# Optimization experiments

Measured on AMD Instinct MI355X. Metric: run time of the kernel, lower is better.

Reference implementation:

```python
import jax, jax.numpy as jnp
import numpy as np

ACT_BITS = 8
W_BITS = 8
C_IN = 64


def round_ste(x):
    # straight-through rounding (Brevitas training behavior)
    return x + jax.lax.stop_gradient(jnp.round(x) - x)


def fake_quant(x, scale, bits, signed):
    if signed:
        lo, hi = -(2 ** (bits - 1)), 2 ** (bits - 1) - 1
    else:
        lo, hi = 0, 2 ** bits - 1
    return jnp.clip(round_ste(x / scale), lo, hi) * scale


def conv_nchw(x, w, pad, groups=1):
    return jax.lax.conv_general_dilated(
        x, w, window_strides=(1, 1), padding=((pad, pad), (pad, pad)),
        dimension_numbers=("NCHW", "OIHW", "NCHW"), feature_group_count=groups)


def setup_inputs() -> dict:
    key = jax.random.key(0)
    k0, k1, k2, k3 = jax.random.split(key, 4)
    x = jax.random.normal(k0, (8, 64, 112, 112), jnp.float32)
    w1 = jax.random.normal(k1, (64, 1, 3, 3), jnp.float32) * 0.05    # depthwise 3x3
    w2 = jax.random.normal(k2, (128, 64, 1, 1), jnp.float32) * 0.05  # pointwise 1x1
    w_sc = jax.random.normal(k3, (128, 64, 1, 1), jnp.float32) * 0.05  # shortcut 1x1
    sc = lambda v: jnp.asarray(v, jnp.float32)
    return dict(x=x, w1=w1, w2=w2, w_sc=w_sc,
                s_in=sc(0.03), s_relu=sc(0.02), s_add=sc(0.03),
                sw1=sc(0.004), sw2=sc(0.004), sw_sc=sc(0.004))


def reference(x, w1, w2, w_sc, s_in, s_relu, s_add, sw1, sw2, sw_sc):
    # quant_input: signed 8-bit fake-quant of the activation
    xq = fake_quant(x, s_in, ACT_BITS, True)
    # shortcut: 1x1 conv with int8 fake-quantized weights (inplane != ouplane)
    identity = conv_nchw(xq, fake_quant(w_sc, sw_sc, W_BITS, True), pad=0)
    # conv1: depthwise 3x3 (groups=inplane) with int8 fake-quantized weights
    y = conv_nchw(xq, fake_quant(w1, sw1, W_BITS, True), pad=1, groups=C_IN)
    # relu2: QuantReLU -> unsigned 8-bit fake-quant of relu
    y = fake_quant(jax.nn.relu(y), s_relu, ACT_BITS, False)
    # conv2: pointwise 1x1
    y = conv_nchw(y, fake_quant(w2, sw2, W_BITS, True), pad=0)
    # residual_add: add then requantize to signed 8-bit
    return fake_quant(y + identity, s_add, ACT_BITS, True)
```

## Files before the change

kernel.cpp:

```cpp
#include <hip/hip_runtime.h>
#include <hip/hip_bf16.h>
#include <stdint.h>

#define NIMG 8
#define CIN  64
#define HWI  12544
#define NP   100352
#define COUT 128

typedef short v8s __attribute__((ext_vector_type(8)));
typedef float v4f __attribute__((ext_vector_type(4)));

static __device__ __forceinline__ int q8(float x, float inv, float lo, float hi) {
    float t = rintf(x * inv);
    t = fminf(fmaxf(t, lo), hi);
    return (int)t;
}

static __device__ __forceinline__ uint32_t funnel(uint32_t hi, uint32_t lo, int sh) {
    return (uint32_t)(((((uint64_t)hi) << 32) | (uint64_t)lo) >> sh);
}

static __device__ __forceinline__ int dot4(uint32_t a, uint32_t b, int c) {
    int acc = c;
    #pragma unroll
    for (int i = 0; i < 4; ++i)
        acc += (int)(int8_t)(a >> (8*i)) * (int)(int8_t)(b >> (8*i));
    return acc;
}

static __device__ __forceinline__ uint16_t i2bf(int v) {
    union { float f; uint32_t u; } c; c.f = (float)v;
    return (uint16_t)(c.u >> 16);
}

__global__ void __launch_bounds__(256) wprep_kernel(
    const float* __restrict__ w2, const float* __restrict__ wsc,
    const float* __restrict__ sw2p, const float* __restrict__ swscp,
    uint16_t* __restrict__ wbuf)
{
    int t = blockIdx.x * 256 + threadIdx.x;
    int f = t * 4;
    int co = f >> 6, k = f & 63;
    float inv2 = 1.0f / sw2p[0];
    float invs = 1.0f / swscp[0];
    float4 a = *(const float4*)(w2 + f);
    float4 b = *(const float4*)(wsc + f);
    float av[4] = {a.x, a.y, a.z, a.w};
    float bv[4] = {b.x, b.y, b.z, b.w};
    uint16_t* d2 = wbuf + co*128 + k;
    uint16_t* ds = wbuf + co*128 + 64 + k;
    ushort2 p2a = make_ushort2(i2bf(q8(av[0], inv2, -128.f, 127.f)),
                               i2bf(q8(av[1], inv2, -128.f, 127.f)));
    ushort2 p2b = make_ushort2(i2bf(q8(av[2], inv2, -128.f, 127.f)),
                               i2bf(q8(av[3], inv2, -128.f, 127.f)));
    ushort2 psa = make_ushort2(i2bf(q8(bv[0], invs, -128.f, 127.f)),
                               i2bf(q8(bv[1], invs, -128.f, 127.f)));
    ushort2 psb = make_ushort2(i2bf(q8(bv[2], invs, -128.f, 127.f)),
                               i2bf(q8(bv[3], invs, -128.f, 127.f)));
    *(ushort2*)(d2)     = p2a;  *(ushort2*)(d2 + 2) = p2b;
    *(ushort2*)(ds)     = psa;  *(ushort2*)(ds + 2) = psb;
}

__global__ void __launch_bounds__(256) dwq_kernel(
    const float* __restrict__ x, const float* __restrict__ w1,
    const float* __restrict__ sinp, const float* __restrict__ srelup,
    const float* __restrict__ sw1p,
    uint16_t* __restrict__ act)
{
    __shared__ int8_t tile[64 * 468];
    int bid = blockIdx.x;
    int n = bid / 56, ht = bid - n*56, hb = ht*2;
    int tid = threadIdx.x;
    float sin_f = sinp[0];
    float inv_sin = 1.0f / sin_f;

    for (int i = 0; i < 28; ++i) {
        int id = tid + i*256;
        int c = id / 112; int rem = id - c*112;
        int r = rem / 28; int seg = rem - r*28;
        int grow = hb + r - 1;
        float4 v = make_float4(0.f, 0.f, 0.f, 0.f);
        if ((unsigned)grow < 112u)
            v = *(const float4*)(x + ((size_t)(n*64 + c) * HWI + grow*112 + seg*4));
        float vv[4] = {v.x, v.y, v.z, v.w};
        uint32_t pk = 0;
        #pragma unroll
        for (int e = 0; e < 4; ++e) {
            int q = q8(vv[e], inv_sin, -128.0f, 127.0f);
            pk |= (uint32_t)(q & 255) << (8*e);
        }
        *(uint32_t*)&tile[c*468 + r*116 + seg*4] = pk;
    }
    {
        int c = tid >> 2, r = tid & 3;
        *(uint32_t*)&tile[c*468 + r*116 + 112] = 0;
    }
    __syncthreads();

    int wave = tid >> 6, lane = tid & 63;
    int rsel = wave >> 1;
    int row  = hb + rsel;
    int half = wave & 1;
    int c = lane;

    float isw1 = 1.0f / sw1p[0];
    uint32_t wp[3];
    #pragma unroll
    for (int ky = 0; ky < 3; ++ky) {
        uint32_t pk = 0;
        #pragma unroll
        for (int kx = 0; kx < 3; ++kx) {
            int q = q8(w1[c*9 + ky*3 + kx], isw1, -128.0f, 127.0f);
            pk |= (uint32_t)(q & 255) << (8*kx);
        }
        wp[ky] = pk;
    }
    float r1 = (sin_f * sw1p[0]) / srelup[0];

    int base[3];
    #pragma unroll
    for (int r2 = 0; r2 < 3; ++r2) base[r2] = c*468 + (rsel + r2)*116;
    int w0b = 56*half;

    uint32_t Ar[3], Br[3], Cr[3];
    #pragma unroll
    for (int r2 = 0; r2 < 3; ++r2) {
        Ar[r2] = half ? *(uint32_t*)&tile[base[r2] + w0b - 4] : 0u;
        Br[r2] = *(uint32_t*)&tile[base[r2] + w0b];
        Cr[r2] = *(uint32_t*)&tile[base[r2] + w0b + 4];
    }
    size_t pbase = (size_t)n*HWI + (size_t)row*112 + w0b;

    for (int q = 0; q < 14; ++q) {
        int acc0 = 0, acc1 = 0, acc2 = 0, acc3 = 0;
        #pragma unroll
        for (int r2 = 0; r2 < 3; ++r2) {
            uint32_t d0 = funnel(Br[r2], Ar[r2], 24);
            uint32_t d1 = Br[r2];
            uint32_t d2 = funnel(Cr[r2], Br[r2], 8);
            uint32_t d3 = funnel(Cr[r2], Br[r2], 16);
            acc0 = dot4(d0, wp[r2], acc0);
            acc1 = dot4(d1, wp[r2], acc1);
            acc2 = dot4(d2, wp[r2], acc2);
            acc3 = dot4(d3, wp[r2], acc3);
        }
        int accs[4] = {acc0, acc1, acc2, acc3};
        uint32_t xdw = Br[1];
        uint16_t* ap = act + (pbase + (size_t)q*4)*128 + c;
        #pragma unroll
        for (int j = 0; j < 4; ++j) {
            float t = rintf((float)accs[j] * r1);
            t = fminf(fmaxf(t, 0.0f), 255.0f);
            int xv = (int)(int8_t)((xdw >> (8*j)) & 255);
            ap[(size_t)j*128]      = i2bf((int)t);
            ap[(size_t)j*128 + 64] = i2bf(xv);
        }
        #pragma unroll
        for (int r2 = 0; r2 < 3; ++r2) { Ar[r2] = Br[r2]; Br[r2] = Cr[r2]; }
        if (q < 13) {
            #pragma unroll
            for (int r2 = 0; r2 < 3; ++r2)
                Cr[r2] = *(uint32_t*)&tile[base[r2] + w0b + q*4 + 8];
        }
    }
}

__global__ void __launch_bounds__(256) gemm_kernel(
    const uint16_t* __restrict__ act, const uint16_t* __restrict__ wbuf,
    const float* __restrict__ sinp, const float* __restrict__ srelup,
    const float* __restrict__ saddp, const float* __restrict__ sw2p,
    const float* __restrict__ swscp,
    float* __restrict__ out)
{
    int bid = blockIdx.x;
    int tid = threadIdx.x;
    int wave = tid >> 6, lane = tid & 63;
    int lr = lane >> 4, ln = lane & 15;
    int p0 = bid * 128;
    int nimg = bid / 98;
    int hw0 = (bid - nimg*98) * 128;

    float S2  = sw2p[0] * srelup[0];
    float Ssc = swscp[0] * sinp[0];
    float sadd = saddp[0];
    float inv_sadd = 1.0f / sadd;

    v8s a[2][4];
    #pragma unroll
    for (int mi = 0; mi < 2; ++mi) {
        int m = (wave*2 + mi)*16 + ln;
        #pragma unroll
        for (int seg = 0; seg < 4; ++seg)
            a[mi][seg] = *(const v8s*)(wbuf + (size_t)m*128 + seg*32 + lr*8);
    }

    for (int nt = 0; nt < 8; ++nt) {
        const uint16_t* bp = act + (size_t)(p0 + nt*16 + ln)*128 + lr*8;
        v8s bf[4];
        #pragma unroll
        for (int seg = 0; seg < 4; ++seg)
            bf[seg] = *(const v8s*)(bp + seg*32);
        int px = hw0 + nt*16 + ln;
        #pragma unroll
        for (int mi = 0; mi < 2; ++mi) {
            v4f acc2 = {0.f, 0.f, 0.f, 0.f};
            v4f accs = {0.f, 0.f, 0.f, 0.f};
            acc2 = __builtin_amdgcn_mfma_f32_16x16x32_bf16(a[mi][0], bf[0], acc2, 0, 0, 0);
            acc2 = __builtin_amdgcn_mfma_f32_16x16x32_bf16(a[mi][1], bf[1], acc2, 0, 0, 0);
            accs = __builtin_amdgcn_mfma_f32_16x16x32_bf16(a[mi][2], bf[2], accs, 0, 0, 0);
            accs = __builtin_amdgcn_mfma_f32_16x16x32_bf16(a[mi][3], bf[3], accs, 0, 0, 0);
            size_t obase = ((size_t)nimg*COUT + (size_t)(wave*2 + mi)*16 + lr*4) * HWI + px;
            #pragma unroll
            for (int r = 0; r < 4; ++r) {
                float v = S2 * acc2[r] + Ssc * accs[r];
                float t = rintf(v * inv_sadd);
                t = fminf(fmaxf(t, -128.0f), 127.0f);
                out[obase + (size_t)r*HWI] = t * sadd;
            }
        }
    }
}

extern "C" void kernel_launch(void* const* d_in, const int* in_sizes, int n_in,
                              void* d_out, int out_size, void* d_ws, size_t ws_size,
                              hipStream_t stream) {
    const float* x     = (const float*)d_in[0];
    const float* w1    = (const float*)d_in[1];
    const float* w2    = (const float*)d_in[2];
    const float* wsc   = (const float*)d_in[3];
    const float* sin   = (const float*)d_in[4];
    const float* srelu = (const float*)d_in[5];
    const float* sadd  = (const float*)d_in[6];
    const float* sw1   = (const float*)d_in[7];
    const float* sw2   = (const float*)d_in[8];
    const float* swsc  = (const float*)d_in[9];

    uint16_t* actb = (uint16_t*)d_ws;
    uint16_t* wbuf = actb + (size_t)NP * 128;

    wprep_kernel<<<8, 256, 0, stream>>>(w2, wsc, sw2, swsc, wbuf);
    dwq_kernel<<<NIMG * 56, 256, 0, stream>>>(x, w1, sin, srelu, sw1, actb);
    gemm_kernel<<<NP / 128, 256, 0, stream>>>(actb, wbuf,
                                              sin, srelu, sadd, sw2, swsc,
                                              (float*)d_out);
}
```

Baseline: 135.2 us.

## Fuse depthwise quant conv and pointwise GEMM into one kernel via LDS

Merges the depthwise 3x3 quantized conv kernel and the 1x1 MFMA GEMM kernel into a single kernel. The int8 activations and the input for each two-row tile are kept in shared memory and converted to bf16 on the fly. This removes the round trip of the large bf16 intermediate activation buffer through global memory. In exchange, shared-memory use per block roughly doubles and the grid is smaller, which reduces occupancy and load balance.

```diff
diff --git a/kernel.cpp b/kernel.cpp
--- a/kernel.cpp
+++ b/kernel.cpp
@@ -50,28 +50,31 @@
     float bv[4] = {b.x, b.y, b.z, b.w};
     uint16_t* d2 = wbuf + co*128 + k;
     uint16_t* ds = wbuf + co*128 + 64 + k;
-    ushort2 p2a = make_ushort2(i2bf(q8(av[0], inv2, -128.f, 127.f)),
-                               i2bf(q8(av[1], inv2, -128.f, 127.f)));
-    ushort2 p2b = make_ushort2(i2bf(q8(av[2], inv2, -128.f, 127.f)),
-                               i2bf(q8(av[3], inv2, -128.f, 127.f)));
-    ushort2 psa = make_ushort2(i2bf(q8(bv[0], invs, -128.f, 127.f)),
-                               i2bf(q8(bv[1], invs, -128.f, 127.f)));
-    ushort2 psb = make_ushort2(i2bf(q8(bv[2], invs, -128.f, 127.f)),
-                               i2bf(q8(bv[3], invs, -128.f, 127.f)));
-    *(ushort2*)(d2)     = p2a;  *(ushort2*)(d2 + 2) = p2b;
-    *(ushort2*)(ds)     = psa;  *(ushort2*)(ds + 2) = psb;
-}
-
-__global__ void __launch_bounds__(256) dwq_kernel(
+    *(ushort2*)(d2)     = make_ushort2(i2bf(q8(av[0], inv2, -128.f, 127.f)),
+                                       i2bf(q8(av[1], inv2, -128.f, 127.f)));
+    *(ushort2*)(d2 + 2) = make_ushort2(i2bf(q8(av[2], inv2, -128.f, 127.f)),
+                                       i2bf(q8(av[3], inv2, -128.f, 127.f)));
+    *(ushort2*)(ds)     = make_ushort2(i2bf(q8(bv[0], invs, -128.f, 127.f)),
+                                       i2bf(q8(bv[1], invs, -128.f, 127.f)));
+    *(ushort2*)(ds + 2) = make_ushort2(i2bf(q8(bv[2], invs, -128.f, 127.f)),
+                                       i2bf(q8(bv[3], invs, -128.f, 127.f)));
+}
+
+__global__ void __launch_bounds__(256) fused_kernel(
     const float* __restrict__ x, const float* __restrict__ w1,
+    const uint16_t* __restrict__ wbuf,
     const float* __restrict__ sinp, const float* __restrict__ srelup,
-    const float* __restrict__ sw1p,
-    uint16_t* __restrict__ act)
+    const float* __restrict__ saddp, const float* __restrict__ sw1p,
+    const float* __restrict__ sw2p, const float* __restrict__ swscp,
+    float* __restrict__ out)
 {
     __shared__ int8_t tile[64 * 468];
+    __shared__ int8_t Bl[224 * 132];
+
     int bid = blockIdx.x;
     int n = bid / 56, ht = bid - n*56, hb = ht*2;
     int tid = threadIdx.x;
+    int wave = tid >> 6, lane = tid & 63;
     float sin_f = sinp[0];
     float inv_sin = 1.0f / sin_f;
 
@@ -98,125 +101,130 @@
     }
     __syncthreads();
 
-    int wave = tid >> 6, lane = tid & 63;
-    int rsel = wave >> 1;
-    int row  = hb + rsel;
-    int half = wave & 1;
-    int c = lane;
-
-    float isw1 = 1.0f / sw1p[0];
-    uint32_t wp[3];
-    #pragma unroll
-    for (int ky = 0; ky < 3; ++ky) {
-        uint32_t pk = 0;
-        #pragma unroll
-        for (int kx = 0; kx < 3; ++kx) {
-            int q = q8(w1[c*9 + ky*3 + kx], isw1, -128.0f, 127.0f);
-            pk |= (uint32_t)(q & 255) << (8*kx);
-        }
-        wp[ky] = pk;
-    }
-    float r1 = (sin_f * sw1p[0]) / srelup[0];
-
-    int base[3];
-    #pragma unroll
-    for (int r2 = 0; r2 < 3; ++r2) base[r2] = c*468 + (rsel + r2)*116;
-    int w0b = 56*half;
-
-    uint32_t Ar[3], Br[3], Cr[3];
-    #pragma unroll
-    for (int r2 = 0; r2 < 3; ++r2) {
-        Ar[r2] = half ? *(uint32_t*)&tile[base[r2] + w0b - 4] : 0u;
-        Br[r2] = *(uint32_t*)&tile[base[r2] + w0b];
-        Cr[r2] = *(uint32_t*)&tile[base[r2] + w0b + 4];
-    }
-    size_t pbase = (size_t)n*HWI + (size_t)row*112 + w0b;
-
-    for (int q = 0; q < 14; ++q) {
-        int acc0 = 0, acc1 = 0, acc2 = 0, acc3 = 0;
+    {
+        int rsel = wave >> 1;
+        int half = wave & 1;
+        int c = lane;
+
+        float isw1 = 1.0f / sw1p[0];
+        uint32_t wp[3];
+        #pragma unroll
+        for (int ky = 0; ky < 3; ++ky) {
+            uint32_t pk = 0;
+            #pragma unroll
+            for (int kx = 0; kx < 3; ++kx) {
+                int q = q8(w1[c*9 + ky*3 + kx], isw1, -128.0f, 127.0f);
+                pk |= (uint32_t)(q & 255) << (8*kx);
+            }
+            wp[ky] = pk;
+        }
+        float r1 = (sin_f * sw1p[0]) / srelup[0];
+
+        int base[3];
+        #pragma unroll
+        for (int r2 = 0; r2 < 3; ++r2) base[r2] = c*468 + (rsel + r2)*116;
+        int w0b = 56*half;
+
+        uint32_t Ar[3], Br[3], Cr[3];
         #pragma unroll
         for (int r2 = 0; r2 < 3; ++r2) {
-            uint32_t d0 = funnel(Br[r2], Ar[r2], 24);
-            uint32_t d1 = Br[r2];
-            uint32_t d2 = funnel(Cr[r2], Br[r2], 8);
-            uint32_t d3 = funnel(Cr[r2], Br[r2], 16);
-            acc0 = dot4(d0, wp[r2], acc0);
-            acc1 = dot4(d1, wp[r2], acc1);
-            acc2 = dot4(d2, wp[r2], acc2);
-            acc3 = dot4(d3, wp[r2], acc3);
-        }
-        int accs[4] = {acc0, acc1, acc2, acc3};
-        uint32_t xdw = Br[1];
-        uint16_t* ap = act + (pbase + (size_t)q*4)*128 + c;
-        #pragma unroll
-        for (int j = 0; j < 4; ++j) {
-            float t = rintf((float)accs[j] * r1);
-            t = fminf(fmaxf(t, 0.0f), 255.0f);
-            int xv = (int)(int8_t)((xdw >> (8*j)) & 255);
-            ap[(size_t)j*128]      = i2bf((int)t);
-            ap[(size_t)j*128 + 64] = i2bf(xv);
-        }
-        #pragma unroll
-        for (int r2 = 0; r2 < 3; ++r2) { Ar[r2] = Br[r2]; Br[r2] = Cr[r2]; }
-        if (q < 13) {
-            #pragma unroll
-            for (int r2 = 0; r2 < 3; ++r2)
-                Cr[r2] = *(uint32_t*)&tile[base[r2] + w0b + q*4 + 8];
-        }
-    }
-}
-
-__global__ void __launch_bounds__(256) gemm_kernel(
-    const uint16_t* __restrict__ act, const uint16_t* __restrict__ wbuf,
-    const float* __restrict__ sinp, const float* __restrict__ srelup,
-    const float* __restrict__ saddp, const float* __restrict__ sw2p,
-    const float* __restrict__ swscp,
-    float* __restrict__ out)
-{
-    int bid = blockIdx.x;
-    int tid = threadIdx.x;
-    int wave = tid >> 6, lane = tid & 63;
-    int lr = lane >> 4, ln = lane & 15;
-    int p0 = bid * 128;
-    int nimg = bid / 98;
-    int hw0 = (bid - nimg*98) * 128;
-
-    float S2  = sw2p[0] * srelup[0];
-    float Ssc = swscp[0] * sinp[0];
-    float sadd = saddp[0];
-    float inv_sadd = 1.0f / sadd;
-
-    v8s a[2][4];
-    #pragma unroll
-    for (int mi = 0; mi < 2; ++mi) {
-        int m = (wave*2 + mi)*16 + ln;
-        #pragma unroll
-        for (int seg = 0; seg < 4; ++seg)
-            a[mi][seg] = *(const v8s*)(wbuf + (size_t)m*128 + seg*32 + lr*8);
-    }
-
-    for (int nt = 0; nt < 8; ++nt) {
-        const uint16_t* bp = act + (size_t)(p0 + nt*16 + ln)*128 + lr*8;
-        v8s bf[4];
-        #pragma unroll
-        for (int seg = 0; seg < 4; ++seg)
-            bf[seg] = *(const v8s*)(bp + seg*32);
-        int px = hw0 + nt*16 + ln;
+            Ar[r2] = half ? *(uint32_t*)&tile[base[r2] + w0b - 4] : 0u;
+            Br[r2] = *(uint32_t*)&tile[base[r2] + w0b];
+            Cr[r2] = *(uint32_t*)&tile[base[r2] + w0b + 4];
+        }
+
+        for (int q = 0; q < 14; ++q) {
+            int acc0 = 0, acc1 = 0, acc2 = 0, acc3 = 0;
+            #pragma unroll
+            for (int r2 = 0; r2 < 3; ++r2) {
+                uint32_t d0 = funnel(Br[r2], Ar[r2], 24);
+                uint32_t d1 = Br[r2];
+                uint32_t d2 = funnel(Cr[r2], Br[r2], 8);
+                uint32_t d3 = funnel(Cr[r2], Br[r2], 16);
+                acc0 = dot4(d0, wp[r2], acc0);
+                acc1 = dot4(d1, wp[r2], acc1);
+                acc2 = dot4(d2, wp[r2], acc2);
+                acc3 = dot4(d3, wp[r2], acc3);
+            }
+            int accs[4] = {acc0, acc1, acc2, acc3};
+            uint32_t xdw = Br[1];
+            int pxb = rsel*112 + w0b + q*4;
+            #pragma unroll
+            for (int j = 0; j < 4; ++j) {
+                float t = rintf((float)accs[j] * r1);
+                t = fminf(fmaxf(t, 0.0f), 255.0f);
+                Bl[(pxb + j)*132 + c]      = (int8_t)(int)t;
+                Bl[(pxb + j)*132 + 64 + c] = (int8_t)((xdw >> (8*j)) & 255);
+            }
+            #pragma unroll
+            for (int r2 = 0; r2 < 3; ++r2) { Ar[r2] = Br[r2]; Br[r2] = Cr[r2]; }
+            if (q < 13) {
+                #pragma unroll
+                for (int r2 = 0; r2 < 3; ++r2)
+                    Cr[r2] = *(uint32_t*)&tile[base[r2] + w0b + q*4 + 8];
+            }
+        }
+    }
+    __syncthreads();
+
+    {
+        int lr = lane >> 4, ln = lane & 15;
+
+        float S2  = sw2p[0] * srelup[0];
+        float Ssc = swscp[0] * sinp[0];
+        float sadd = saddp[0];
+        float inv_sadd = 1.0f / sadd;
+
+        v8s a[2][4];
         #pragma unroll
         for (int mi = 0; mi < 2; ++mi) {
-            v4f acc2 = {0.f, 0.f, 0.f, 0.f};
-            v4f accs = {0.f, 0.f, 0.f, 0.f};
-            acc2 = __builtin_amdgcn_mfma_f32_16x16x32_bf16(a[mi][0], bf[0], acc2, 0, 0, 0);
-            acc2 = __builtin_amdgcn_mfma_f32_16x16x32_bf16(a[mi][1], bf[1], acc2, 0, 0, 0);
-            accs = __builtin_amdgcn_mfma_f32_16x16x32_bf16(a[mi][2], bf[2], accs, 0, 0, 0);
-            accs = __builtin_amdgcn_mfma_f32_16x16x32_bf16(a[mi][3], bf[3], accs, 0, 0, 0);
-            size_t obase = ((size_t)nimg*COUT + (size_t)(wave*2 + mi)*16 + lr*4) * HWI + px;
-            #pragma unroll
-            for (int r = 0; r < 4; ++r) {
-                float v = S2 * acc2[r] + Ssc * accs[r];
-                float t = rintf(v * inv_sadd);
-                t = fminf(fmaxf(t, -128.0f), 127.0f);
-                out[obase + (size_t)r*HWI] = t * sadd;
+            int m = (wave*2 + mi)*16 + ln;
+            #pragma unroll
+            for (int seg = 0; seg < 4; ++seg)
+                a[mi][seg] = *(const v8s*)(wbuf + (size_t)m*128 + seg*32 + lr*8);
+        }
+
+        size_t orow = (size_t)n*COUT*HWI + (size_t)hb*112;
+
+        for (int nt = 0; nt < 14; ++nt) {
+            int boff = (nt*16 + ln)*132 + lr*8;
+            v8s bf[4];
+            #pragma unroll
+            for (int seg = 0; seg < 4; ++seg) {
+                uint32_t d0 = *(const uint32_t*)&Bl[boff + seg*32];
+                uint32_t d1 = *(const uint32_t*)&Bl[boff + seg*32 + 4];
+                v8s t;
+                if (seg < 2) {
+                    #pragma unroll
+                    for (int e = 0; e < 4; ++e) {
+                        t[e]     = (short)i2bf((int)((d0 >> (8*e)) & 255u));
+                        t[4 + e] = (short)i2bf((int)((d1 >> (8*e)) & 255u));
+                    }
+                } else {
+                    #pragma unroll
+                    for (int e = 0; e < 4; ++e) {
+                        t[e]     = (short)i2bf((int)(int8_t)(d0 >> (8*e)));
+                        t[4 + e] = (short)i2bf((int)(int8_t)(d1 >> (8*e)));
+                    }
+                }
+                bf[seg] = t;
+            }
+            #pragma unroll
+            for (int mi = 0; mi < 2; ++mi) {
+                v4f acc2 = {0.f, 0.f, 0.f, 0.f};
+                v4f accs = {0.f, 0.f, 0.f, 0.f};
+                acc2 = __builtin_amdgcn_mfma_f32_16x16x32_bf16(a[mi][0], bf[0], acc2, 0, 0, 0);
+                acc2 = __builtin_amdgcn_mfma_f32_16x16x32_bf16(a[mi][1], bf[1], acc2, 0, 0, 0);
+                accs = __builtin_amdgcn_mfma_f32_16x16x32_bf16(a[mi][2], bf[2], accs, 0, 0, 0);
+                accs = __builtin_amdgcn_mfma_f32_16x16x32_bf16(a[mi][3], bf[3], accs, 0, 0, 0);
+                size_t obase = orow + (size_t)((wave*2 + mi)*16 + lr*4)*HWI + nt*16 + ln;
+                #pragma unroll
+                for (int r = 0; r < 4; ++r) {
+                    float v = S2 * acc2[r] + Ssc * accs[r];
+                    float t = rintf(v * inv_sadd);
+                    t = fminf(fmaxf(t, -128.0f), 127.0f);
+                    out[obase + (size_t)r*HWI] = t * sadd;
+                }
             }
         }
     }
@@ -236,12 +244,10 @@
     const float* sw2   = (const float*)d_in[8];
     const float* swsc  = (const float*)d_in[9];
 
-    uint16_t* actb = (uint16_t*)d_ws;
-    uint16_t* wbuf = actb + (size_t)NP * 128;
+    uint16_t* wbuf = (uint16_t*)d_ws;
 
     wprep_kernel<<<8, 256, 0, stream>>>(w2, wsc, sw2, swsc, wbuf);
-    dwq_kernel<<<NIMG * 56, 256, 0, stream>>>(x, w1, sin, srelu, sw1, actb);
-    gemm_kernel<<<NP / 128, 256, 0, stream>>>(actb, wbuf,
-                                              sin, srelu, sadd, sw2, swsc,
-                                              (float*)d_out);
-}
+    fused_kernel<<<NIMG * 56, 256, 0, stream>>>(x, w1, wbuf,
+                                                sin, srelu, sadd, sw1, sw2, swsc,
+                                                (float*)d_out);
+}
```

Result: faster. 120.9 us (-10.5%).
